# Optimization experiments

Measured on AMD Instinct MI355X. Metric: run time of the kernel, lower is better.

Reference implementation:

```python
import jax, jax.numpy as jnp
import numpy as np

DIM = 384
NUM_HEADS = 12
WIN = 7
N = WIN * WIN  # 49
B = 4096


def _relative_position_index():
    coords = np.stack(np.meshgrid(np.arange(WIN), np.arange(WIN), indexing='ij'))  # (2,W,W)
    cf = coords.reshape(2, -1)  # (2, N)
    rel = cf[:, :, None] - cf[:, None, :]  # (2, N, N)
    rel = rel.transpose(1, 2, 0).astype(np.int64)  # (N, N, 2)
    rel[:, :, 0] += WIN - 1
    rel[:, :, 1] += WIN - 1
    rel[:, :, 0] *= 2 * WIN - 1
    return jnp.asarray(rel.sum(-1), dtype=jnp.int32)  # (N, N)


def setup_inputs() -> dict:
    key = jax.random.key(0)
    ks = jax.random.split(key, 6)
    x = jax.random.normal(ks[0], (B, N, DIM), dtype=jnp.float32)
    mask = jnp.zeros((B, N, N), dtype=jnp.float32)
    qkv_w = jax.random.normal(ks[1], (3 * DIM, DIM), dtype=jnp.float32) * 0.02
    qkv_b = jnp.zeros((3 * DIM,), dtype=jnp.float32)
    proj_w = jax.random.normal(ks[2], (DIM, DIM), dtype=jnp.float32) * 0.02
    proj_b = jnp.zeros((DIM,), dtype=jnp.float32)
    bias_table = jax.random.normal(ks[3], ((2 * WIN - 1) ** 2, NUM_HEADS), dtype=jnp.float32) * 0.02
    rel_index = _relative_position_index()
    return {"x": x, "mask": mask, "qkv_w": qkv_w, "qkv_b": qkv_b,
            "proj_w": proj_w, "proj_b": proj_b, "bias_table": bias_table,
            "rel_index": rel_index}


def reference(x, mask, qkv_w, qkv_b, proj_w, proj_b, bias_table, rel_index):
    B_, n, C = x.shape
    H = NUM_HEADS
    d = C // H
    scale = d ** (-0.5)
    # fused qkv projection: (B_, n, 3, H, d)
    qkv = (x @ qkv_w.T + qkv_b).reshape(B_, n, 3, H, d)
    qkv = jnp.transpose(qkv, (2, 0, 3, 1, 4))  # (3, B_, H, n, d)
    q, k, v = qkv[0], qkv[1], qkv[2]
    attn = jnp.einsum('bhnd,bhmd->bhnm', q * scale, k)  # (B_, H, n, n)
    # relative position bias gather: (n, n, H) -> (H, n, n)
    rel_bias = jnp.transpose(bias_table[rel_index], (2, 0, 1))
    attn = attn + rel_bias[None] + mask[:, None]
    attn = jax.nn.softmax(attn, axis=-1)
    out = jnp.einsum('bhnm,bhmd->bnhd', attn, v).reshape(B_, n, C)
    return out @ proj_w.T + proj_b
```

## Files before the change

kernel.cpp:

```cpp
#include <hip/hip_runtime.h>
#include <hip/hip_bf16.h>

#define NWIN   4096
#define NTOK   49
#define CDIM   384
#define NHEAD  12
#define QKVN   1152
#define SLICE  1568
#define MPROW  28

typedef __attribute__((ext_vector_type(8))) short bf16x8;
typedef __attribute__((ext_vector_type(4))) short bf16x4;
typedef __attribute__((ext_vector_type(4))) float f32x4;
typedef __attribute__((ext_vector_type(2))) unsigned int u32x2;
typedef unsigned int u32;
typedef unsigned short u16;

static __device__ __forceinline__ u16 f2bf(float f) {
  union { float f; u32 u; } w; w.f = f;
  u32 r = w.u + 0x7fffu + ((w.u >> 16) & 1u);
  return (u16)(r >> 16);
}
static __device__ __forceinline__ float blo(u32 v) {
  union { u32 u; float f; } w; w.u = v << 16; return w.f;
}
static __device__ __forceinline__ float bhi(u32 v) {
  union { u32 u; float f; } w; w.u = v & 0xffff0000u; return w.f;
}
static __device__ __forceinline__ u32 cvtpk2(float lo, float hi) {
  u32 r; asm("v_cvt_pk_bf16_f32 %0, %1, %2" : "=v"(r) : "v"(lo), "v"(hi));
  return r;
}
static __device__ __forceinline__ void gld_lds16(const u16* g, u16* l) {
  __builtin_amdgcn_global_load_lds((const __attribute__((address_space(1))) u32*)g,
                                   (__attribute__((address_space(3))) u32*)l, 16, 0, 0);
}

__global__ void k_prep(const float* __restrict__ qkv_w, const float* __restrict__ proj_w,
                       const float* __restrict__ btab, const int* __restrict__ ridx,
                       const float* __restrict__ mask,
                       u16* __restrict__ wq, u16* __restrict__ wp, u32* __restrict__ rbp,
                       u32* __restrict__ mpk)
{
  const int n1 = QKVN * CDIM;
  const int n2 = CDIM * CDIM;
  const int n3 = NHEAD * NTOK * 26;
  const int n4 = NWIN * NTOK * MPROW;
  for (int i = blockIdx.x * blockDim.x + threadIdx.x; i < n1 + n2 + n3 + n4;
       i += gridDim.x * blockDim.x) {
    if (i < n1) {
      wq[i] = f2bf(qkv_w[i]);
    } else if (i < n1 + n2) {
      wp[i - n1] = f2bf(proj_w[i - n1]);
    } else if (i < n1 + n2 + n3) {
      int t = i - n1 - n2;
      int h = t / (NTOK * 26); int rem = t % (NTOK * 26);
      int r = rem / 26, p = rem % 26;
      float lo = 0.f, hi = 0.f;
      if (p < 25) {
        lo = btab[ridx[r * NTOK + 2 * p] * NHEAD + h];
        if (2 * p + 1 < NTOK) hi = btab[ridx[r * NTOK + 2 * p + 1] * NHEAD + h];
      }
      rbp[(h * NTOK + r) * 26 + p] = (u32)f2bf(lo) | ((u32)f2bf(hi) << 16);
    } else {
      int t2 = i - n1 - n2 - n3;
      int wi = t2 / MPROW, p = t2 - wi * MPROW;
      u32 v = 0;
      if (p < 25) {
        const float* mrow = mask + (long)wi * NTOK;
        float lo = mrow[2 * p];
        float hi = (2 * p + 1 < NTOK) ? mrow[2 * p + 1] : 0.f;
        v = (u32)f2bf(lo) | ((u32)f2bf(hi) << 16);
      }
      mpk[t2] = v;
    }
  }
}

__global__ void k_convx(const float* __restrict__ x, u16* __restrict__ xb, long n8)
{
  long i = (long)blockIdx.x * blockDim.x + threadIdx.x;
  long stride = (long)gridDim.x * blockDim.x;
  for (; i < n8; i += stride) {
    const float4* p = (const float4*)x + i * 2;
    float4 a = p[0], b = p[1];
    u32 w0 = (u32)f2bf(a.x) | ((u32)f2bf(a.y) << 16);
    u32 w1 = (u32)f2bf(a.z) | ((u32)f2bf(a.w) << 16);
    u32 w2 = (u32)f2bf(b.x) | ((u32)f2bf(b.y) << 16);
    u32 w3 = (u32)f2bf(b.z) | ((u32)f2bf(b.w) << 16);
    uint4 v; v.x = w0; v.y = w1; v.z = w2; v.w = w3;
    ((uint4*)xb)[i] = v;
  }
}

template<bool OUT_SLICE>
__global__ __launch_bounds__(256, 4)
void k_gemm(const u16* __restrict__ A, int lda,
            const u16* __restrict__ Bt, const float* __restrict__ bias,
            void* __restrict__ C, int ldc, int K, int tiles_n)
{
  __shared__ alignas(16) u16 As[128 * 64];
  __shared__ alignas(16) u16 Bs[128 * 64];
  const int tid = threadIdx.x;
  const int w = tid >> 6, l = tid & 63;

  const int nwg = (int)gridDim.x;
  const int xcd = (int)blockIdx.x & 7, idx8 = (int)blockIdx.x >> 3;
  const int q8 = nwg >> 3, r8w = nwg & 7;
  const int lid = (xcd < r8w ? xcd * (q8 + 1) : r8w * (q8 + 1) + (xcd - r8w) * q8) + idx8;

  const int tm = lid / tiles_n, tn = lid % tiles_n;
  const int wm = (w >> 1) * 64, wn = (w & 1) * 64;
  const long arow0 = (long)tm * 128;
  const long brow0 = (long)tn * 128;
  const int r8 = l >> 3;
  const int c8 = ((l & 7) ^ r8) * 8;

  f32x4 acc[4][4];
  const f32x4 z = {0.f, 0.f, 0.f, 0.f};
#pragma unroll
  for (int m = 0; m < 4; ++m)
#pragma unroll
    for (int n = 0; n < 4; ++n) acc[m][n] = z;

  for (int kk = 0; kk < K; kk += 64) {
    __syncthreads();
#pragma unroll
    for (int q = 0; q < 4; ++q) {
      int ra = w * 32 + q * 8;
      gld_lds16(A  + (arow0 + ra + r8) * (long)lda + kk + c8, &As[ra * 64]);
      gld_lds16(Bt + (brow0 + ra + r8) * (long)K   + kk + c8, &Bs[ra * 64]);
    }
    __syncthreads();
#pragma unroll
    for (int ks = 0; ks < 2; ++ks) {
      const int ko = ks * 32 + (l >> 4) * 8;
      const int rl = l & 15;
      const int sa = (rl & 7) * 8;
      bf16x8 af[4], bfr[4];
#pragma unroll
      for (int m = 0; m < 4; ++m) af[m]  = *(const bf16x8*)&As[(wm + m * 16 + rl) * 64 + (ko ^ sa)];
#pragma unroll
      for (int n = 0; n < 4; ++n) bfr[n] = *(const bf16x8*)&Bs[(wn + n * 16 + rl) * 64 + (ko ^ sa)];
#pragma unroll
      for (int m = 0; m < 4; ++m)
#pragma unroll
        for (int n = 0; n < 4; ++n)
          acc[m][n] = __builtin_amdgcn_mfma_f32_16x16x32_bf16(bfr[n], af[m], acc[m][n], 0, 0, 0);
    }
  }

  const int li = l & 15, g4 = (l >> 4) * 4;
  float4 bv[4];
#pragma unroll
  for (int n = 0; n < 4; ++n)
    bv[n] = *(const float4*)&bias[tn * 128 + wn + n * 16 + g4];
#pragma unroll
  for (int m = 0; m < 4; ++m) {
    const int row = (int)arow0 + wm + m * 16 + li;
    const int b = (int)(((unsigned long long)(unsigned)row * 342393ull) >> 24);
    const int tok = row - b * 49;
#pragma unroll
    for (int n = 0; n < 4; ++n) {
      float v0 = acc[m][n][0] + bv[n].x;
      float v1 = acc[m][n][1] + bv[n].y;
      float v2 = acc[m][n][2] + bv[n].z;
      float v3 = acc[m][n][3] + bv[n].w;
      const int col = (int)brow0 + wn + n * 16 + g4;
      if (OUT_SLICE) {
        const int t = (col >= 768) ? 2 : ((col >= 384) ? 1 : 0);
        const int rem = col - t * 384;
        const int hh = rem >> 5, d = rem & 31;
        const long dst = (((long)b * NHEAD + hh) * 3 + t) * SLICE + tok * 32 + d;
        u32x2 pk;
        pk[0] = (u32)f2bf(v0) | ((u32)f2bf(v1) << 16);
        pk[1] = (u32)f2bf(v2) | ((u32)f2bf(v3) << 16);
        *(u32x2*)((u16*)C + dst) = pk;
      } else {
        float4 pk; pk.x = v0; pk.y = v1; pk.z = v2; pk.w = v3;
        *(float4*)((float*)C + (long)row * ldc + col) = pk;
      }
    }
  }
}

__global__ __launch_bounds__(256, 4)
void k_attn(const u16* __restrict__ qkv, u16* __restrict__ ob,
            const u32* __restrict__ mpk, const u32* __restrict__ rbp)
{
  __shared__ alignas(16) u16 Vt[4][32 * 64];
  __shared__ alignas(16) u32 mp[1536];
  const int tid = threadIdx.x;
  const int w = tid >> 6, l = tid & 63;
  const int g = l >> 4, li = l & 15;
  const int id = blockIdx.x;
  const int logical = (id & 7) * ((int)gridDim.x >> 3) + (id >> 3);
  const int bl = logical / 3, hg = logical - bl * 3;
  const int h = hg * 4 + w;
  const long rowbase = (long)bl * NTOK;
  const float scale = 0.17677669529663687f;

  const long sb = ((long)bl * NHEAD + h) * 3 * SLICE;
  const u16* qs = qkv + sb;
  const u16* ks = qs + SLICE;
  const u16* vs = qs + 2 * SLICE;

  bf16x8 kf[4];
#pragma unroll
  for (int jm = 0; jm < 4; ++jm) {
    int rj = jm * 16 + li; if (rj >= NTOK) rj = NTOK - 1;
    kf[jm] = *(const bf16x8*)(ks + rj * 32 + g * 8);
  }
  bf16x8 qfc = *(const bf16x8*)(qs + li * 32 + g * 8);

  u16* vt = Vt[w];
  {
    const int jj = l >> 2;
    const int d0 = (l & 3) * 8;
#pragma unroll
    for (int it = 0; it < 4; ++it) {
      int j = it * 16 + jj;
      bf16x8 vv = {0, 0, 0, 0, 0, 0, 0, 0};
      if (j < NTOK)
        vv = *(const bf16x8*)(vs + j * 32 + d0);
#pragma unroll
      for (int t = 0; t < 8; ++t)
        vt[(d0 + t) * 64 + (j ^ (t << 3))] = (u16)vv[t];
    }
  }
  {
    const u32* mpkb = mpk + (long)bl * (NTOK * MPROW);
    for (int base = w * 1024; base < NTOK * MPROW * 4; base += 4096) {
      int soff = base + l * 16;
      if (soff > NTOK * MPROW * 4 - 16) soff = NTOK * MPROW * 4 - 16;
      gld_lds16((const u16*)((const char*)mpkb + soff), (u16*)((char*)mp + base));
    }
  }
  __syncthreads();

  const int sw = (li & 7) << 3;
  const f32x4 z = {0.f, 0.f, 0.f, 0.f};
  f32x4 oacc[4][2];
#pragma unroll
  for (int im = 0; im < 4; ++im)
#pragma unroll
    for (int dn = 0; dn < 2; ++dn) oacc[im][dn] = z;

#pragma unroll
  for (int in = 0; in < 4; ++in) {
    __builtin_amdgcn_s_setprio(1);
    f32x4 s[4];
#pragma unroll
    for (int jm = 0; jm < 4; ++jm)
      s[jm] = __builtin_amdgcn_mfma_f32_16x16x32_bf16(kf[jm], qfc, z, 0, 0, 0);
    __builtin_amdgcn_s_setprio(0);

    bf16x8 qfn = qfc;
    if (in < 3) {
      int ri = (in + 1) * 16 + li; if (ri >= NTOK) ri = NTOK - 1;
      qfn = *(const bf16x8*)(qs + ri * 32 + g * 8);
    }

    const int i = 16 * in + li;
    const int ic = i < NTOK ? i : NTOK - 1;
#pragma unroll
    for (int jm = 0; jm < 4; ++jm) {
      int p0 = 8 * jm + 2 * g; if (p0 > 24) p0 = 24;
      const u32* bp = rbp + (h * NTOK + ic) * 26 + p0;
      u32 b0w = bp[0], b1w = bp[1];
      u32 m0w = mp[ic * MPROW + p0], m1w = mp[ic * MPROW + p0 + 1];
      s[jm][0] = s[jm][0] * scale + blo(b0w) + blo(m0w);
      s[jm][1] = s[jm][1] * scale + bhi(b0w) + bhi(m0w);
      s[jm][2] = s[jm][2] * scale + blo(b1w) + blo(m1w);
      s[jm][3] = s[jm][3] * scale + bhi(b1w) + bhi(m1w);
    }

    float mx = -3.0e38f;
#pragma unroll
    for (int jm = 0; jm < 4; ++jm)
#pragma unroll
      for (int rr = 0; rr < 4; ++rr) mx = fmaxf(mx, s[jm][rr]);
    mx = fmaxf(mx, __shfl_xor(mx, 16));
    mx = fmaxf(mx, __shfl_xor(mx, 32));
    float sum = 0.f;
#pragma unroll
    for (int jm = 0; jm < 4; ++jm) {
      const int j0 = 16 * jm + 4 * g;
#pragma unroll
      for (int rr = 0; rr < 4; ++rr) {
        float p = (j0 + rr < NTOK) ? __expf(s[jm][rr] - mx) : 0.f;
        s[jm][rr] = p; sum += p;
      }
    }
    sum += __shfl_xor(sum, 16);
    sum += __shfl_xor(sum, 32);
    const float inv = (i < NTOK) ? (1.f / sum) : 0.f;

    __builtin_amdgcn_s_setprio(1);
#pragma unroll
    for (int ks2 = 0; ks2 < 2; ++ks2) {
      union { u32 ww[4]; bf16x8 v8; } pa;
      pa.ww[0] = cvtpk2(s[2 * ks2][0] * inv, s[2 * ks2][1] * inv);
      pa.ww[1] = cvtpk2(s[2 * ks2][2] * inv, s[2 * ks2][3] * inv);
      pa.ww[2] = cvtpk2(s[2 * ks2 + 1][0] * inv, s[2 * ks2 + 1][1] * inv);
      pa.ww[3] = cvtpk2(s[2 * ks2 + 1][2] * inv, s[2 * ks2 + 1][3] * inv);
#pragma unroll
      for (int dn = 0; dn < 2; ++dn) {
        union { bf16x4 hh[2]; bf16x8 v8; } vfr;
        const u16* vrow = &vt[(16 * dn + li) * 64];
        vfr.hh[0] = *(const bf16x4*)&vrow[(32 * ks2 + 4 * g) ^ sw];
        vfr.hh[1] = *(const bf16x4*)&vrow[(32 * ks2 + 16 + 4 * g) ^ sw];
        oacc[in][dn] = __builtin_amdgcn_mfma_f32_16x16x32_bf16(pa.v8, vfr.v8, oacc[in][dn], 0, 0, 0);
      }
    }
    __builtin_amdgcn_s_setprio(0);
    qfc = qfn;
  }

#pragma unroll
  for (int im = 0; im < 4; ++im) {
#pragma unroll
    for (int rr = 0; rr < 4; ++rr) {
      const int i = 16 * im + 4 * g + rr;
      if (i < NTOK) {
        u16* orow = ob + (rowbase + i) * CDIM + h * 32;
#pragma unroll
        for (int dn = 0; dn < 2; ++dn)
          orow[16 * dn + li] = f2bf(oacc[im][dn][rr]);
      }
    }
  }
}

extern "C" void kernel_launch(void* const* d_in, const int* in_sizes, int n_in,
                              void* d_out, int out_size, void* d_ws, size_t ws_size,
                              hipStream_t stream)
{
  const float* x      = (const float*)d_in[0];
  const float* mask   = (const float*)d_in[1];
  const float* qkv_w  = (const float*)d_in[2];
  const float* qkv_b  = (const float*)d_in[3];
  const float* proj_w = (const float*)d_in[4];
  const float* proj_b = (const float*)d_in[5];
  const float* btab   = (const float*)d_in[6];
  const int*   ridx   = (const int*)d_in[7];
  float* out = (float*)d_out;

  const size_t fixed = (size_t)QKVN * CDIM * 2 + (size_t)CDIM * CDIM * 2
                     + (size_t)NHEAD * NTOK * 26 * 4
                     + (size_t)NWIN * NTOK * MPROW * 4 + 1024;
  auto need = [&](int bc) -> size_t {
    return (size_t)bc * NTOK * QKVN * 2
         + (size_t)bc * NTOK * CDIM * 2
         + fixed;
  };
  int BC = NWIN;
  while (BC > 128 && need(BC) > ws_size) BC >>= 1;

  char* p = (char*)d_ws;
  u16* qkvbuf = (u16*)p;  p += (size_t)BC * NTOK * QKVN * 2;
  u16* xb     = (u16*)p;  p += (size_t)BC * NTOK * CDIM * 2;
  u16* wq     = (u16*)p;  p += (size_t)QKVN * CDIM * 2;
  u16* wp     = (u16*)p;  p += (size_t)CDIM * CDIM * 2;
  u32* rbp    = (u32*)p;  p += (size_t)NHEAD * NTOK * 26 * 4;
  u32* mpk    = (u32*)p;

  k_prep<<<512, 256, 0, stream>>>(qkv_w, proj_w, btab, ridx, mask, wq, wp, rbp, mpk);

  const int nc = NWIN / BC;
  const int Mc = BC * NTOK;
  for (int c = 0; c < nc; ++c) {
    const float* xc = x + (size_t)c * Mc * CDIM;
    k_convx<<<2048, 256, 0, stream>>>(xc, xb, (long)Mc * CDIM / 8);
    k_gemm<true><<<(Mc / 128) * 9, 256, 0, stream>>>(
        xb, CDIM, wq, qkv_b, (void*)qkvbuf, QKVN, CDIM, 9);
    k_attn<<<BC * 3, 256, 0, stream>>>(
        qkvbuf, xb, mpk + (size_t)c * BC * NTOK * MPROW, rbp);
    k_gemm<false><<<(Mc / 128) * 3, 256, 0, stream>>>(
        xb, CDIM, wp, proj_b, (void*)(out + (size_t)c * Mc * CDIM), CDIM, CDIM, 3);
  }
}
```

Measured before the change: 685.5 us.

## Write V transposed from QKV GEMM epilogue and load V fragments directly

The QKV GEMM epilogue now stores V in a per-head, d-major layout (row stride 56). The attention kernel can then load its V MFMA operands straight from global memory into registers, dropping the LDS transpose buffer and its scattered 2-byte LDS writes. In exchange, the GEMM writes V as four strided 2-byte stores per thread instead of one packed 8-byte store, which is poorly coalesced. The padding columns of V^T (tokens 49-55) are never written, and fragment reads run past the 56-element row. Those values are multiplied by zero probabilities, so correctness relies on the workspace holding no NaN or Inf there.

```diff
diff --git a/kernel.cpp b/kernel.cpp
--- a/kernel.cpp
+++ b/kernel.cpp
@@ -6,7 +6,9 @@
 #define CDIM   384
 #define NHEAD  12
 #define QKVN   1152
-#define SLICE  1568
+#define QKSL   1568
+#define VTSL   1792
+#define HSL    4928
 #define MPROW  28
 
 typedef __attribute__((ext_vector_type(8))) short bf16x8;
@@ -171,11 +173,20 @@
         const int t = (col >= 768) ? 2 : ((col >= 384) ? 1 : 0);
         const int rem = col - t * 384;
         const int hh = rem >> 5, d = rem & 31;
-        const long dst = (((long)b * NHEAD + hh) * 3 + t) * SLICE + tok * 32 + d;
-        u32x2 pk;
-        pk[0] = (u32)f2bf(v0) | ((u32)f2bf(v1) << 16);
-        pk[1] = (u32)f2bf(v2) | ((u32)f2bf(v3) << 16);
-        *(u32x2*)((u16*)C + dst) = pk;
+        const long hb = ((long)b * NHEAD + hh) * HSL;
+        if (t == 2) {
+          u16* vp = (u16*)C + hb + 2 * QKSL + tok;
+          vp[(long)(d + 0) * 56] = f2bf(v0);
+          vp[(long)(d + 1) * 56] = f2bf(v1);
+          vp[(long)(d + 2) * 56] = f2bf(v2);
+          vp[(long)(d + 3) * 56] = f2bf(v3);
+        } else {
+          const long dst = hb + (long)t * QKSL + tok * 32 + d;
+          u32x2 pk;
+          pk[0] = (u32)f2bf(v0) | ((u32)f2bf(v1) << 16);
+          pk[1] = (u32)f2bf(v2) | ((u32)f2bf(v3) << 16);
+          *(u32x2*)((u16*)C + dst) = pk;
+        }
       } else {
         float4 pk; pk.x = v0; pk.y = v1; pk.z = v2; pk.w = v3;
         *(float4*)((float*)C + (long)row * ldc + col) = pk;
@@ -188,7 +199,6 @@
 void k_attn(const u16* __restrict__ qkv, u16* __restrict__ ob,
             const u32* __restrict__ mpk, const u32* __restrict__ rbp)
 {
-  __shared__ alignas(16) u16 Vt[4][32 * 64];
   __shared__ alignas(16) u32 mp[1536];
   const int tid = threadIdx.x;
   const int w = tid >> 6, l = tid & 63;
@@ -200,10 +210,10 @@
   const long rowbase = (long)bl * NTOK;
   const float scale = 0.17677669529663687f;
 
-  const long sb = ((long)bl * NHEAD + h) * 3 * SLICE;
-  const u16* qs = qkv + sb;
-  const u16* ks = qs + SLICE;
-  const u16* vs = qs + 2 * SLICE;
+  const long hb = ((long)bl * NHEAD + h) * HSL;
+  const u16* qs  = qkv + hb;
+  const u16* ks  = qs + QKSL;
+  const u16* vts = qs + 2 * QKSL;
 
   bf16x8 kf[4];
 #pragma unroll
@@ -212,22 +222,16 @@
     kf[jm] = *(const bf16x8*)(ks + rj * 32 + g * 8);
   }
   bf16x8 qfc = *(const bf16x8*)(qs + li * 32 + g * 8);
-
-  u16* vt = Vt[w];
-  {
-    const int jj = l >> 2;
-    const int d0 = (l & 3) * 8;
-#pragma unroll
-    for (int it = 0; it < 4; ++it) {
-      int j = it * 16 + jj;
-      bf16x8 vv = {0, 0, 0, 0, 0, 0, 0, 0};
-      if (j < NTOK)
-        vv = *(const bf16x8*)(vs + j * 32 + d0);
-#pragma unroll
-      for (int t = 0; t < 8; ++t)
-        vt[(d0 + t) * 64 + (j ^ (t << 3))] = (u16)vv[t];
-    }
-  }
+  union { bf16x4 hh[2]; bf16x8 v8; } vf[2][2];
+#pragma unroll
+  for (int ks2 = 0; ks2 < 2; ++ks2)
+#pragma unroll
+    for (int dn = 0; dn < 2; ++dn) {
+      const u16* vrow = vts + (16 * dn + li) * 56;
+      vf[ks2][dn].hh[0] = *(const bf16x4*)&vrow[32 * ks2 + 4 * g];
+      vf[ks2][dn].hh[1] = *(const bf16x4*)&vrow[32 * ks2 + 16 + 4 * g];
+    }
+
   {
     const u32* mpkb = mpk + (long)bl * (NTOK * MPROW);
     for (int base = w * 1024; base < NTOK * MPROW * 4; base += 4096) {
@@ -238,7 +242,6 @@
   }
   __syncthreads();
 
-  const int sw = (li & 7) << 3;
   const f32x4 z = {0.f, 0.f, 0.f, 0.f};
   f32x4 oacc[4][2];
 #pragma unroll
@@ -305,13 +308,8 @@
       pa.ww[2] = cvtpk2(s[2 * ks2 + 1][0] * inv, s[2 * ks2 + 1][1] * inv);
       pa.ww[3] = cvtpk2(s[2 * ks2 + 1][2] * inv, s[2 * ks2 + 1][3] * inv);
 #pragma unroll
-      for (int dn = 0; dn < 2; ++dn) {
-        union { bf16x4 hh[2]; bf16x8 v8; } vfr;
-        const u16* vrow = &vt[(16 * dn + li) * 64];
-        vfr.hh[0] = *(const bf16x4*)&vrow[(32 * ks2 + 4 * g) ^ sw];
-        vfr.hh[1] = *(const bf16x4*)&vrow[(32 * ks2 + 16 + 4 * g) ^ sw];
-        oacc[in][dn] = __builtin_amdgcn_mfma_f32_16x16x32_bf16(pa.v8, vfr.v8, oacc[in][dn], 0, 0, 0);
-      }
+      for (int dn = 0; dn < 2; ++dn)
+        oacc[in][dn] = __builtin_amdgcn_mfma_f32_16x16x32_bf16(pa.v8, vf[ks2][dn].v8, oacc[in][dn], 0, 0, 0);
     }
     __builtin_amdgcn_s_setprio(0);
     qfc = qfn;
@@ -350,7 +348,7 @@
                      + (size_t)NHEAD * NTOK * 26 * 4
                      + (size_t)NWIN * NTOK * MPROW * 4 + 1024;
   auto need = [&](int bc) -> size_t {
-    return (size_t)bc * NTOK * QKVN * 2
+    return (size_t)bc * NHEAD * HSL * 2
          + (size_t)bc * NTOK * CDIM * 2
          + fixed;
   };
@@ -358,7 +356,7 @@
   while (BC > 128 && need(BC) > ws_size) BC >>= 1;
 
   char* p = (char*)d_ws;
-  u16* qkvbuf = (u16*)p;  p += (size_t)BC * NTOK * QKVN * 2;
+  u16* qkvbuf = (u16*)p;  p += (size_t)BC * NHEAD * HSL * 2;
   u16* xb     = (u16*)p;  p += (size_t)BC * NTOK * CDIM * 2;
   u16* wq     = (u16*)p;  p += (size_t)QKVN * CDIM * 2;
   u16* wp     = (u16*)p;  p += (size_t)CDIM * CDIM * 2;
```

New measurement: 721.6 us. 5.3% more time.

## Double-buffer LDS tiles in GEMM to overlap global loads with MFMA

Applied to the files above, without the earlier changes.

Doubles the A/B shared-memory tiles in the bf16 GEMM and prefetches the next K-slice into the alternate buffer while the current one feeds the MFMAs. Explicit vmcnt waits and raw barriers replace the two syncthreads per iteration. The goal is to hide global-to-LDS latency behind compute. In exchange LDS use doubles to 64KB and the launch bound drops to 2 blocks per CU, which lowers occupancy.

```diff
diff --git a/kernel.cpp b/kernel.cpp
--- a/kernel.cpp
+++ b/kernel.cpp
@@ -94,13 +94,13 @@
 }
 
 template<bool OUT_SLICE>
-__global__ __launch_bounds__(256, 4)
+__global__ __launch_bounds__(256, 2)
 void k_gemm(const u16* __restrict__ A, int lda,
             const u16* __restrict__ Bt, const float* __restrict__ bias,
             void* __restrict__ C, int ldc, int K, int tiles_n)
 {
-  __shared__ alignas(16) u16 As[128 * 64];
-  __shared__ alignas(16) u16 Bs[128 * 64];
+  __shared__ alignas(16) u16 As[2][128 * 64];
+  __shared__ alignas(16) u16 Bs[2][128 * 64];
   const int tid = threadIdx.x;
   const int w = tid >> 6, l = tid & 63;
 
@@ -116,6 +116,15 @@
   const int r8 = l >> 3;
   const int c8 = ((l & 7) ^ r8) * 8;
 
+  auto stage = [&](int kk, int buf) {
+#pragma unroll
+    for (int q = 0; q < 4; ++q) {
+      int ra = w * 32 + q * 8;
+      gld_lds16(A  + (arow0 + ra + r8) * (long)lda + kk + c8, &As[buf][ra * 64]);
+      gld_lds16(Bt + (brow0 + ra + r8) * (long)K   + kk + c8, &Bs[buf][ra * 64]);
+    }
+  };
+
   f32x4 acc[4][4];
   const f32x4 z = {0.f, 0.f, 0.f, 0.f};
 #pragma unroll
@@ -123,15 +132,18 @@
 #pragma unroll
     for (int n = 0; n < 4; ++n) acc[m][n] = z;
 
+  stage(0, 0);
+  int cur = 0;
   for (int kk = 0; kk < K; kk += 64) {
-    __syncthreads();
-#pragma unroll
-    for (int q = 0; q < 4; ++q) {
-      int ra = w * 32 + q * 8;
-      gld_lds16(A  + (arow0 + ra + r8) * (long)lda + kk + c8, &As[ra * 64]);
-      gld_lds16(Bt + (brow0 + ra + r8) * (long)K   + kk + c8, &Bs[ra * 64]);
-    }
-    __syncthreads();
+    if (kk + 64 < K) {
+      stage(kk + 64, cur ^ 1);
+      asm volatile("s_waitcnt vmcnt(8)" ::: "memory");
+    } else {
+      asm volatile("s_waitcnt vmcnt(0)" ::: "memory");
+    }
+    __builtin_amdgcn_sched_barrier(0);
+    __builtin_amdgcn_s_barrier();
+    __builtin_amdgcn_sched_barrier(0);
 #pragma unroll
     for (int ks = 0; ks < 2; ++ks) {
       const int ko = ks * 32 + (l >> 4) * 8;
@@ -139,15 +151,19 @@
       const int sa = (rl & 7) * 8;
       bf16x8 af[4], bfr[4];
 #pragma unroll
-      for (int m = 0; m < 4; ++m) af[m]  = *(const bf16x8*)&As[(wm + m * 16 + rl) * 64 + (ko ^ sa)];
-#pragma unroll
-      for (int n = 0; n < 4; ++n) bfr[n] = *(const bf16x8*)&Bs[(wn + n * 16 + rl) * 64 + (ko ^ sa)];
+      for (int m = 0; m < 4; ++m) af[m]  = *(const bf16x8*)&As[cur][(wm + m * 16 + rl) * 64 + (ko ^ sa)];
+#pragma unroll
+      for (int n = 0; n < 4; ++n) bfr[n] = *(const bf16x8*)&Bs[cur][(wn + n * 16 + rl) * 64 + (ko ^ sa)];
 #pragma unroll
       for (int m = 0; m < 4; ++m)
 #pragma unroll
         for (int n = 0; n < 4; ++n)
           acc[m][n] = __builtin_amdgcn_mfma_f32_16x16x32_bf16(bfr[n], af[m], acc[m][n], 0, 0, 0);
     }
+    __builtin_amdgcn_sched_barrier(0);
+    __builtin_amdgcn_s_barrier();
+    __builtin_amdgcn_sched_barrier(0);
+    cur ^= 1;
   }
 
   const int li = l & 15, g4 = (l >> 4) * 4;
```

Result: slower. 768.0 us (+12.0%).
